# Optimization experiments

Hardware: AMD Instinct MI355X
Metric: run time of the kernel (lower is better)

The kernel has to match this reference:

```python
import jax, jax.numpy as jnp
import numpy as np

B, T, H, N = 2, 1024, 32, 64
HN = H * N              # 2048 hidden size
KVH, KVD = 8, 512       # GQA kv heads / kv width; repeat = HN // KVD = 4
LW, LA, LV, LG, LK = 64, 64, 32, 128, 32   # wavgk_split_list
EPS = 1e-6

def _rms(x, w):
    xf = x.astype(jnp.float32)
    var = jnp.mean(xf * xf, axis=-1, keepdims=True)
    return (w * (xf * jax.lax.rsqrt(var + EPS))).astype(x.dtype)

def _rot_half(x):
    x1, x2 = jnp.split(x, 2, axis=-1)
    return jnp.concatenate([-x2, x1], axis=-1)

def setup_inputs():
    key = jax.random.key(0)
    ks = iter(jax.random.split(key, 32))
    nrm = lambda s, sc=1.0: jax.random.normal(next(ks), s, jnp.float32) * sc
    d = {
        'x_in': nrm((B, T, HN)),
        'v_first': nrm((B, T, KVH, N)),
        'k_first': nrm((B, T, KVH, N)),
        'state': jnp.zeros((B, H, N, N), jnp.float32),
    }
    pos = jnp.arange(T, dtype=jnp.float32)
    inv = 1.0 / (10000.0 ** (jnp.arange(0, N, 2, dtype=jnp.float32) / N))
    ang = pos[:, None] * inv[None, :]
    ang = jnp.concatenate([ang, ang], axis=-1)   # [T, N]
    d['calc_cos'] = jnp.broadcast_to(jnp.cos(ang), (B, T, N))
    d['calc_sin'] = jnp.broadcast_to(jnp.sin(ang), (B, T, N))
    d.update(
        wavgk1=nrm((HN, LW + LA + LV + LG + LK), 0.02),
        w0=jnp.zeros((HN,), jnp.float32), w2=nrm((LW, HN), 0.02),
        a0=jnp.zeros((HN,), jnp.float32), a2=nrm((LA, HN), 0.02),
        v0=jnp.zeros((KVD,), jnp.float32), v2=nrm((LV, KVD), 0.02),
        g2=nrm((LG, HN), 0.02),
        k0=jnp.zeros((KVD,), jnp.float32), k2=nrm((LK, KVD), 0.02),
        r_k=nrm((H, N), 0.1),
        RKV_w=nrm((HN + 2 * KVD, HN), 0.02),
        O_w=nrm((HN, HN), 0.02),
        R_bias=jnp.zeros((HN,), jnp.float32),
        K_bias=jnp.zeros((KVD,), jnp.float32),
        V_bias=jnp.zeros((KVD,), jnp.float32),
        O_bias=jnp.zeros((HN,), jnp.float32),
        ln_r=jnp.ones((N,), jnp.float32),
        ln_k=jnp.ones((N,), jnp.float32),
        ln1=jnp.ones((HN,), jnp.float32),
    )
    return d

def reference(x_in, v_first, k_first, state, calc_cos, calc_sin, wavgk1, w0, w2,
              a0, a2, v0, v2, g2, k0, k2, r_k, RKV_w, O_w, R_bias, K_bias,
              V_bias, O_bias, ln_r, ln_k, ln1):
    rep = HN // KVD
    x = _rms(x_in, ln1)
    rkv = x @ RKV_w.T                                   # dense form of fpx_matmul
    r, k, v = jnp.split(rkv, [HN, HN + KVD], axis=-1)
    xw, xa, xv, xg, xk = jnp.split(x @ wavgk1, [LW, LW + LA, LW + LA + LV, LW + LA + LV + LG], axis=-1)
    r = r + R_bias; k = k + K_bias; v = v + V_bias
    r = _rms(r.reshape(B, T, H, N), ln_r)
    k = _rms(k.reshape(B, T, KVH, N), ln_k)
    cos, sin = calc_cos[:, :, None, :], calc_sin[:, :, None, :]   # unsqueeze_dim=2
    r = r * cos + _rot_half(r) * sin
    k = k * cos + _rot_half(k) * sin
    v = v.reshape(B, T, KVH, N)
    # layer_id > 0 path: gated residual toward layer-0 v/k
    gate_v = jax.nn.sigmoid(xv @ v2 + v0).reshape(B, T, KVH, N)
    v = v + (v_first - v) * gate_v
    gate_k = jax.nn.sigmoid(xk @ k2 + k0).reshape(B, T, KVH, N)
    k = k + (k_first - k) * gate_k
    w = jnp.tanh(xw) @ w2 + w0
    w = -jax.nn.softplus(-w) - 0.5
    # GQA repeat kv heads to H
    k = jnp.broadcast_to(k[:, :, :, None, :], (B, T, KVH, rep, N)).reshape(B, T, HN)
    v = jnp.broadcast_to(v[:, :, :, None, :], (B, T, KVH, rep, N)).reshape(B, T, HN)
    r = r.reshape(B, T, HN)
    a = jax.nn.sigmoid(xa @ a2 + a0)
    g = jax.nn.sigmoid(xg) @ g2
    kh = k.reshape(B, T, H, N)
    kk = (kh / jnp.maximum(jnp.linalg.norm(kh, axis=-1, keepdims=True), 1e-12)).reshape(B, T, HN)
    k = k * (1.0 - w + a)
    aa, bb = -kk, kk * a
    w = -jnp.exp(w.astype(jnp.float32))                 # log-decay (negative)
    # RWKV-7 recurrence: S <- S*diag(exp(w)) + (S a) b^T + v k^T ; o = S r
    hv = lambda t: jnp.moveaxis(t.reshape(B, T, H, N).astype(jnp.float32), 1, 0)
    def step(S, ts):
        r_t, w_t, k_t, v_t, a_t, b_t = ts               # each [B,H,N]
        sa = jnp.einsum('bhvk,bhk->bhv', S, a_t)
        S = S * jnp.exp(w_t)[:, :, None, :] + sa[..., None] * b_t[:, :, None, :] + v_t[..., None] * k_t[:, :, None, :]
        return S, jnp.einsum('bhvk,bhk->bhv', S, r_t)
    _, o = jax.lax.scan(step, state.astype(jnp.float32), (hv(r), hv(w), hv(k), hv(v), hv(aa), hv(bb)))
    xx = jnp.moveaxis(o, 0, 1).reshape(B, T, HN) * float(N) ** -0.5
    r_, k_, v_ = (t.reshape(B, T, H, N) for t in (r, k, v))
    bonus = (jnp.sum(r_ * k_ * r_k, axis=-1, keepdims=True) * v_).reshape(B, T, HN)
    xx = xx.astype(x_in.dtype) + bonus
    return x_in + (xx * g) @ O_w.T + O_bias
```

## Files before the change

### kernel.cpp

```cpp
#include <hip/hip_runtime.h>
#include <hip/hip_bf16.h>
#include <stdint.h>

#define B_ 2
#define T_ 1024
#define H_ 32
#define N_ 64
#define HN_ 2048
#define KVH_ 8
#define KVD_ 512
#define MTOK 2048
#define SMN 7168
#define KCAT 320
#define CH 64
#define NCH 16
#define NCHUNK 1024

typedef __bf16 bf16x8 __attribute__((ext_vector_type(8)));
typedef float f32x4 __attribute__((ext_vector_type(4)));

typedef __attribute__((address_space(1))) uint32_t gu32;
typedef __attribute__((address_space(3))) uint32_t lu32;
__device__ __forceinline__ void gload16(const void* g, void* l) {
    __builtin_amdgcn_global_load_lds((gu32*)g, (lu32*)l, 16, 0, 0);
}

__device__ __forceinline__ float sigmf(float x) { return 1.f / (1.f + expf(-x)); }

#define PREP_N1 (3072 * 2048)
#define PREP_N2 (2048 * 2048)
#define PREP_N3 (320 * 2048)
#define PREP_N4 (SMN * KCAT)
__global__ void prep_kernel(const float* __restrict__ RKV_w, const float* __restrict__ O_w,
                            const float* __restrict__ wavgk1,
                            const float* __restrict__ w2, const float* __restrict__ a2,
                            const float* __restrict__ v2, const float* __restrict__ g2,
                            const float* __restrict__ k2,
                            __hip_bfloat16* __restrict__ RKVb, __hip_bfloat16* __restrict__ OWb,
                            __hip_bfloat16* __restrict__ WT1b, __hip_bfloat16* __restrict__ Wcatb) {
    long i = (long)blockIdx.x * 256 + threadIdx.x;
    if (i < PREP_N1) { RKVb[i] = __float2bfloat16(RKV_w[i]); return; }
    i -= PREP_N1;
    if (i < PREP_N2) { OWb[i] = __float2bfloat16(O_w[i]); return; }
    i -= PREP_N2;
    if (i < PREP_N3) {
        int c = (int)(i / 2048), r = (int)(i % 2048);
        WT1b[i] = __float2bfloat16(wavgk1[(size_t)r * 320 + c]);
        return;
    }
    i -= PREP_N3;
    if (i >= PREP_N4) return;
    int j = (int)(i / KCAT), k = (int)(i % KCAT);
    float v = 0.f;
    if (j < 2048)      { if (k < 64)             v = w2[(size_t)k * 2048 + j]; }
    else if (j < 4096) { if (k >= 64 && k < 128)  v = a2[(size_t)(k - 64) * 2048 + (j - 2048)]; }
    else if (j < 4608) { if (k >= 128 && k < 160) v = v2[(size_t)(k - 128) * 512 + (j - 4096)]; }
    else if (j < 6656) { if (k >= 160 && k < 288) v = g2[(size_t)(k - 160) * 2048 + (j - 4608)]; }
    else               { if (k >= 288)            v = k2[(size_t)(k - 288) * 512 + (j - 6656)]; }
    Wcatb[i] = __float2bfloat16(v);
}

__global__ __launch_bounds__(256) void rmsnorm_kernel(const float* __restrict__ x,
                                                      const float* __restrict__ ln1,
                                                      __hip_bfloat16* __restrict__ out) {
    const int bt = blockIdx.x, tid = threadIdx.x;
    const float* row = x + (size_t)bt * HN_;
    float4 v0 = *(const float4*)(row + tid * 8);
    float4 v1 = *(const float4*)(row + tid * 8 + 4);
    float s = v0.x*v0.x + v0.y*v0.y + v0.z*v0.z + v0.w*v0.w
            + v1.x*v1.x + v1.y*v1.y + v1.z*v1.z + v1.w*v1.w;
    for (int m = 1; m < 64; m <<= 1) s += __shfl_xor(s, m);
    __shared__ float red[4];
    if ((tid & 63) == 0) red[tid >> 6] = s;
    __syncthreads();
    s = red[0] + red[1] + red[2] + red[3];
    float scale = rsqrtf(s * (1.f / HN_) + 1e-6f);
    float vals[8] = {v0.x, v0.y, v0.z, v0.w, v1.x, v1.y, v1.z, v1.w};
    #pragma unroll
    for (int j = 0; j < 8; ++j)
        out[(size_t)bt * HN_ + tid * 8 + j] = __float2bfloat16(vals[j] * scale * ln1[tid * 8 + j]);
}

__global__ __launch_bounds__(256) void gemm_xw_sk(const __hip_bfloat16* __restrict__ A,
                                                  const __hip_bfloat16* __restrict__ B,
                                                  float* __restrict__ Cp, int M, int N, int K) {
    __shared__ __align__(16) __hip_bfloat16 As[64][40];
    __shared__ __align__(16) __hip_bfloat16 Bs[64][40];
    const int tid = threadIdx.x;
    const int wave = tid >> 6, lane = tid & 63;
    const int wr = (wave >> 1) * 32, wc = (wave & 1) * 32;
    const int brow = blockIdx.y << 6, bcol = blockIdx.x << 6;
    const int z = blockIdx.z;
    const int kbeg = z * (K >> 2), kend = kbeg + (K >> 2);
    const int lrow = tid >> 2, lcol = (tid & 3) << 3;
    const int fr = lane & 15, ko = (lane >> 4) << 3;
    f32x4 acc[2][2] = {};
    for (int k0 = kbeg; k0 < kend; k0 += 32) {
        uint4 av = *(const uint4*)(A + (size_t)(brow + lrow) * K + k0 + lcol);
        uint4 bv = *(const uint4*)(B + (size_t)(bcol + lrow) * K + k0 + lcol);
        *(uint4*)(&As[lrow][lcol]) = av;
        *(uint4*)(&Bs[lrow][lcol]) = bv;
        __syncthreads();
        bf16x8 af0 = *(const bf16x8*)(&As[wr + fr][ko]);
        bf16x8 af1 = *(const bf16x8*)(&As[wr + 16 + fr][ko]);
        bf16x8 bf0 = *(const bf16x8*)(&Bs[wc + fr][ko]);
        bf16x8 bf1 = *(const bf16x8*)(&Bs[wc + 16 + fr][ko]);
        acc[0][0] = __builtin_amdgcn_mfma_f32_16x16x32_bf16(af0, bf0, acc[0][0], 0, 0, 0);
        acc[0][1] = __builtin_amdgcn_mfma_f32_16x16x32_bf16(af0, bf1, acc[0][1], 0, 0, 0);
        acc[1][0] = __builtin_amdgcn_mfma_f32_16x16x32_bf16(af1, bf0, acc[1][0], 0, 0, 0);
        acc[1][1] = __builtin_amdgcn_mfma_f32_16x16x32_bf16(af1, bf1, acc[1][1], 0, 0, 0);
        __syncthreads();
    }
    const int cr = (lane >> 4) << 2, cc = lane & 15;
    float* Cz = Cp + (size_t)z * M * N;
    #pragma unroll
    for (int i = 0; i < 2; ++i)
        #pragma unroll
        for (int j = 0; j < 2; ++j)
            #pragma unroll
            for (int r = 0; r < 4; ++r) {
                int row = brow + wr + i * 16 + cr + r;
                int col = bcol + wc + j * 16 + cc;
                Cz[(size_t)row * N + col] = acc[i][j][r];
            }
}

__global__ void xw_reduce(const float* __restrict__ Cp, __hip_bfloat16* __restrict__ out) {
    long i = (long)blockIdx.x * 256 + threadIdx.x;
    if (i >= (long)MTOK * KCAT) return;
    const long MN = (long)MTOK * KCAT;
    float v = Cp[i] + Cp[i + MN] + Cp[i + 2 * MN] + Cp[i + 3 * MN];
    int c = (int)(i % KCAT);
    if (c < 64) v = tanhf(v);
    else if (c >= 160 && c < 288) v = sigmf(v);
    out[i] = __float2bfloat16(v);
}

__global__ __launch_bounds__(256) void gemm_bt128(const __hip_bfloat16* __restrict__ A,
                                                  const __hip_bfloat16* __restrict__ B,
                                                  float* __restrict__ C, int M, int N, int K,
                                                  const float* __restrict__ bias,
                                                  const float* __restrict__ addend) {
    __shared__ __align__(16) __hip_bfloat16 As[128][32];
    __shared__ __align__(16) __hip_bfloat16 Bs[128][32];
    const int tid = threadIdx.x;
    const int wave = tid >> 6, lane = tid & 63;
    const int wr = (wave >> 1) * 64, wc = (wave & 1) * 64;
    const int brow = blockIdx.y << 7, bcol = blockIdx.x << 7;
    const int fr = lane & 15, ko = (lane >> 4) << 3;
    const int ar0 = wave * 32;
    const int sr = lane >> 2;
    const int sc = (lane & 3) << 3;
    f32x4 acc[4][4] = {};
    const __hip_bfloat16* gA0 = A + (size_t)(brow + ar0 + sr) * K + sc;
    const __hip_bfloat16* gA1 = A + (size_t)(brow + ar0 + 16 + sr) * K + sc;
    const __hip_bfloat16* gB0 = B + (size_t)(bcol + ar0 + sr) * K + sc;
    const __hip_bfloat16* gB1 = B + (size_t)(bcol + ar0 + 16 + sr) * K + sc;
    for (int k0 = 0; k0 < K; k0 += 32) {
        gload16(gA0 + k0, &As[ar0][0]);
        gload16(gA1 + k0, &As[ar0 + 16][0]);
        gload16(gB0 + k0, &Bs[ar0][0]);
        gload16(gB1 + k0, &Bs[ar0 + 16][0]);
        __syncthreads();
        bf16x8 af[4], bfr[4];
        #pragma unroll
        for (int i = 0; i < 4; ++i) {
            af[i]  = *(const bf16x8*)(&As[wr + i * 16 + fr][ko]);
            bfr[i] = *(const bf16x8*)(&Bs[wc + i * 16 + fr][ko]);
        }
        #pragma unroll
        for (int i = 0; i < 4; ++i)
            #pragma unroll
            for (int j = 0; j < 4; ++j)
                acc[i][j] = __builtin_amdgcn_mfma_f32_16x16x32_bf16(af[i], bfr[j], acc[i][j], 0, 0, 0);
        __syncthreads();
    }
    const int cr = (lane >> 4) << 2, cc = lane & 15;
    #pragma unroll
    for (int i = 0; i < 4; ++i)
        #pragma unroll
        for (int j = 0; j < 4; ++j) {
            const int row0 = brow + wr + i * 16 + cr;
            const int col = bcol + wc + j * 16 + cc;
            #pragma unroll
            for (int r = 0; r < 4; ++r) {
                float v = acc[i][j][r];
                if (bias) v += bias[col];
                if (addend) v += addend[(size_t)(row0 + r) * N + col];
                C[(size_t)(row0 + r) * N + col] = v;
            }
        }
}

__global__ __launch_bounds__(256) void compose_kernel(
    const float* __restrict__ RKV, const float* __restrict__ SM,
    const float* __restrict__ v_first, const float* __restrict__ k_first,
    const float* __restrict__ cosd, const float* __restrict__ sind,
    const float* __restrict__ R_bias, const float* __restrict__ K_bias,
    const float* __restrict__ V_bias, const float* __restrict__ w0,
    const float* __restrict__ a0, const float* __restrict__ v0b,
    const float* __restrict__ k0b, const float* __restrict__ ln_r,
    const float* __restrict__ ln_k, const float* __restrict__ r_k,
    char* __restrict__ SC, __hip_bfloat16* __restrict__ VB, float* __restrict__ SB,
    __hip_bfloat16* __restrict__ G) {
    __shared__ __align__(16) float rbuf[HN_];
    __shared__ __align__(16) float kbuf[KVD_];
    __shared__ __align__(16) float vbuf[KVD_];
    __shared__ float knorms[KVH_];
    __shared__ float cosb[64], sinb[64];
    const int bt = blockIdx.x;
    const int b = bt >> 10, t = bt & 1023;
    const int tid = threadIdx.x;
    const float* rkvrow = RKV + (size_t)bt * 3072;
    const float* smrow = SM + (size_t)bt * SMN;

    if (tid < 64) {
        cosb[tid] = cosd[(size_t)bt * 64 + tid];
        sinb[tid] = sind[(size_t)bt * 64 + tid];
    }

    const int h = tid >> 3;
    const int off = (tid & 7) << 3;
    const int n0 = tid << 3;
    float rraw[8];
    {
        float4 x0 = *(const float4*)(rkvrow + n0);
        float4 x1 = *(const float4*)(rkvrow + n0 + 4);
        float4 b0 = *(const float4*)(R_bias + n0);
        float4 b1 = *(const float4*)(R_bias + n0 + 4);
        rraw[0] = x0.x + b0.x; rraw[1] = x0.y + b0.y; rraw[2] = x0.z + b0.z; rraw[3] = x0.w + b0.w;
        rraw[4] = x1.x + b1.x; rraw[5] = x1.y + b1.y; rraw[6] = x1.z + b1.z; rraw[7] = x1.w + b1.w;
    }
    float rss = 0.f;
    #pragma unroll
    for (int j = 0; j < 8; ++j) { rss += rraw[j] * rraw[j]; rbuf[n0 + j] = rraw[j]; }
    rss += __shfl_xor(rss, 1); rss += __shfl_xor(rss, 2); rss += __shfl_xor(rss, 4);
    float rscale = rsqrtf(rss * (1.f / 64.f) + 1e-6f);

    const int kvh = tid >> 5;
    const int ko2 = (tid & 31) << 1;
    const int kidx = kvh * 64 + ko2;
    float kraw0 = rkvrow[2048 + kidx] + K_bias[kidx];
    float kraw1 = rkvrow[2048 + kidx + 1] + K_bias[kidx + 1];
    float kss = kraw0 * kraw0 + kraw1 * kraw1;
    kss += __shfl_xor(kss, 1); kss += __shfl_xor(kss, 2); kss += __shfl_xor(kss, 4);
    kss += __shfl_xor(kss, 8); kss += __shfl_xor(kss, 16);
    float kscale = rsqrtf(kss * (1.f / 64.f) + 1e-6f);
    kbuf[kidx] = kraw0; kbuf[kidx + 1] = kraw1;

    {
        float va = rkvrow[2560 + kidx] + V_bias[kidx];
        float vb2 = rkvrow[2560 + kidx + 1] + V_bias[kidx + 1];
        float gv0 = sigmf(smrow[4096 + kidx] + v0b[kidx]);
        float gv1 = sigmf(smrow[4096 + kidx + 1] + v0b[kidx + 1]);
        vbuf[kidx] = va + (v_first[(size_t)bt * 512 + kidx] - va) * gv0;
        vbuf[kidx + 1] = vb2 + (v_first[(size_t)bt * 512 + kidx + 1] - vb2) * gv1;
    }
    __syncthreads();

    float rf[8];
    #pragma unroll
    for (int j = 0; j < 8; ++j) {
        int nn = off + j;
        int nn2 = (nn + 32) & 63;
        float val = rbuf[h * 64 + nn] * rscale * ln_r[nn];
        float oth = rbuf[h * 64 + nn2] * rscale * ln_r[nn2];
        float rot = (nn < 32) ? -oth : oth;
        rf[j] = val * cosb[nn] + rot * sinb[nn];
    }
    float kfv[2];
    #pragma unroll
    for (int j = 0; j < 2; ++j) {
        int nn = ko2 + j;
        int nn2 = (nn + 32) & 63;
        float val = kbuf[kvh * 64 + nn] * kscale * ln_k[nn];
        float oth = kbuf[kvh * 64 + nn2] * kscale * ln_k[nn2];
        float rot = (nn < 32) ? -oth : oth;
        float kr = val * cosb[nn] + rot * sinb[nn];
        float gk = sigmf(smrow[6656 + kvh * 64 + nn] + k0b[kvh * 64 + nn]);
        kfv[j] = kr + (k_first[(size_t)bt * 512 + kvh * 64 + nn] - kr) * gk;
    }
    __syncthreads();
    kbuf[kidx] = kfv[0]; kbuf[kidx + 1] = kfv[1];
    float kn = kfv[0] * kfv[0] + kfv[1] * kfv[1];
    kn += __shfl_xor(kn, 1); kn += __shfl_xor(kn, 2); kn += __shfl_xor(kn, 4);
    kn += __shfl_xor(kn, 8); kn += __shfl_xor(kn, 16);
    if ((tid & 31) == 0) knorms[kvh] = fmaxf(sqrtf(kn), 1e-12f);
    __syncthreads();

    const float knv = knorms[h >> 2];
    char* scb = SC + ((size_t)(b * H_ + h) * T_ + t) * 896;
    __hip_bfloat16* us = (__hip_bfloat16*)scb;
    float* df = (float*)(scb + 640);
    float4 w1a = *(const float4*)(smrow + n0);
    float4 w1b = *(const float4*)(smrow + n0 + 4);
    float4 ara = *(const float4*)(smrow + 2048 + n0);
    float4 arb = *(const float4*)(smrow + 2048 + n0 + 4);
    float4 ga  = *(const float4*)(smrow + 4608 + n0);
    float4 gb  = *(const float4*)(smrow + 4608 + n0 + 4);
    float w1arr[8] = {w1a.x, w1a.y, w1a.z, w1a.w, w1b.x, w1b.y, w1b.z, w1b.w};
    float aarr[8] = {ara.x, ara.y, ara.z, ara.w, arb.x, arb.y, arb.z, arb.w};
    float garr[8] = {ga.x, ga.y, ga.z, ga.w, gb.x, gb.y, gb.z, gb.w};
    float bsum = 0.f;
    #pragma unroll
    for (int j = 0; j < 8; ++j) {
        int nn = off + j, n = n0 + j;
        float w1 = w1arr[j] + w0[n];
        float w2v = -log1pf(expf(-w1)) - 0.5f;
        float av = sigmf(aarr[j] + a0[n]);
        float dec = expf(-expf(w2v));
        float kb = kbuf[(h >> 2) * 64 + nn];
        float vbv = vbuf[(h >> 2) * 64 + nn];
        float kkv = kb / knv;
        float ksc = kb * (1.f - w2v + av);
        us[nn]       = __float2bfloat16(rf[j]);
        us[64 + nn]  = __float2bfloat16(ksc);
        us[128 + nn] = __float2bfloat16(-kkv);
        us[192 + nn] = __float2bfloat16(kkv * av);
        us[256 + nn] = __float2bfloat16(vbv);
        df[nn] = dec;
        VB[(size_t)bt * HN_ + n] = __float2bfloat16(vbv);
        G[(size_t)bt * HN_ + n] = __float2bfloat16(garr[j]);
        bsum += rf[j] * ksc * r_k[h * 64 + nn];
    }
    bsum += __shfl_xor(bsum, 1); bsum += __shfl_xor(bsum, 2); bsum += __shfl_xor(bsum, 4);
    if ((tid & 7) == 0) SB[bt * H_ + h] = bsum;
}

__global__ __launch_bounds__(256) void scan_pass1(
    const char* __restrict__ SC, float* __restrict__ Q, float* __restrict__ O,
    float* __restrict__ Pf, float* __restrict__ Sf) {
    const int chunk = blockIdx.x;
    const int bh = chunk >> 4, c = chunk & 15;
    const int b = bh >> 5, h = bh & 31;
    const int tid = threadIdx.x;
    const int wid = tid >> 6, lane = tid & 63;
    const int cq = lane >> 4;
    const int cb = cq << 4;
    const int row = (wid << 4) + (lane & 15);
    const char* base = SC + ((size_t)bh * T_ + (size_t)c * CH) * 896;
    __shared__ __align__(16) float ld[2][6][64];

    f32x4 P4[4], S4[4];
    #pragma unroll
    for (int j = 0; j < 4; ++j)
        #pragma unroll
        for (int e = 0; e < 4; ++e) {
            P4[j][e] = (cb + 4 * j + e == row) ? 1.f : 0.f;
            S4[j][e] = 0.f;
        }

    float p0 = 0.f, p1 = 0.f;
    auto LOADT = [&](int t) {
        const __hip_bfloat16* us = (const __hip_bfloat16*)(base + (size_t)t * 896);
        if (wid == 0)      { p0 = __bfloat162float(us[128 + lane]); p1 = __bfloat162float(us[lane]); }
        else if (wid == 1) { p0 = __bfloat162float(us[192 + lane]); p1 = __bfloat162float(us[256 + lane]); }
        else if (wid == 2) { p0 = *(const float*)(base + (size_t)t * 896 + 640 + 4 * lane); }
        else               { p0 = __bfloat162float(us[64 + lane]); }
    };
    LOADT(0);
    float* qrow = Q + (size_t)chunk * CH * 64 + row;
    float* orow = O + ((size_t)b * T_ + (size_t)c * CH) * HN_ + h * 64 + row;
    for (int t = 0; t < CH; ++t) {
        const int buf = t & 1;
        if (wid == 0)      { ld[buf][0][lane] = p0; ld[buf][4][lane] = p1; }
        else if (wid == 1) { ld[buf][1][lane] = p0; ld[buf][5][lane] = p1; }
        else if (wid == 2) { ld[buf][2][lane] = p0; }
        else               { ld[buf][3][lane] = p0; }
        __syncthreads();
        if (t + 1 < CH) LOADT(t + 1);
        f32x4 a4[4];
        #pragma unroll
        for (int j = 0; j < 4; ++j) a4[j] = *(const f32x4*)&ld[buf][0][cb + 4 * j];
        f32x4 dpv = {0,0,0,0}, dsv = {0,0,0,0};
        #pragma unroll
        for (int j = 0; j < 4; ++j) { dpv += P4[j] * a4[j]; dsv += S4[j] * a4[j]; }
        float dp = dpv[0] + dpv[1] + dpv[2] + dpv[3];
        float dsd = dsv[0] + dsv[1] + dsv[2] + dsv[3];
        dp += __shfl_xor(dp, 16);  dp += __shfl_xor(dp, 32);
        dsd += __shfl_xor(dsd, 16); dsd += __shfl_xor(dsd, 32);
        const float vt = ld[buf][5][row];
        const f32x4 cPv = {dp, dp, dp, dp}, sav = {dsd, dsd, dsd, dsd}, vtv = {vt, vt, vt, vt};
        f32x4 qp = {0,0,0,0}, op = {0,0,0,0};
        #pragma unroll
        for (int j = 0; j < 4; ++j) {
            f32x4 d4 = *(const f32x4*)&ld[buf][2][cb + 4 * j];
            f32x4 b4 = *(const f32x4*)&ld[buf][1][cb + 4 * j];
            f32x4 k4 = *(const f32x4*)&ld[buf][3][cb + 4 * j];
            f32x4 r4 = *(const f32x4*)&ld[buf][4][cb + 4 * j];
            f32x4 Pn = P4[j] * d4 + cPv * b4;
            f32x4 Sn = S4[j] * d4 + sav * b4 + vtv * k4;
            P4[j] = Pn; S4[j] = Sn;
            qp += Pn * r4; op += Sn * r4;
        }
        float qs = qp[0] + qp[1] + qp[2] + qp[3];
        float os = op[0] + op[1] + op[2] + op[3];
        qs += __shfl_xor(qs, 16); qs += __shfl_xor(qs, 32);
        os += __shfl_xor(os, 16); os += __shfl_xor(os, 32);
        if (cq == 0) {
            qrow[(size_t)t * 64] = qs;
            orow[(size_t)t * HN_] = os;
        }
    }
    float* pf = Pf + (size_t)chunk * 4096 + (size_t)row * 64 + cb;
    float* sf = Sf + (size_t)chunk * 4096 + (size_t)row * 64 + cb;
    #pragma unroll
    for (int j = 0; j < 4; ++j) {
        *(f32x4*)(pf + 4 * j) = P4[j];
        *(f32x4*)(sf + 4 * j) = S4[j];
    }
}

__global__ __launch_bounds__(256) void scan_pass2(
    const float* __restrict__ Pf, float* __restrict__ Sf, const float* __restrict__ state) {
    const int blk = blockIdx.x;
    const int bh = blk >> 2, rb = blk & 3;
    const int tid = threadIdx.x;
    const int lv = tid >> 4, c0 = (tid & 15) << 2;
    __shared__ __align__(16) float S[16][68];
    __shared__ __align__(16) float P[64][64];

    *(f32x4*)&S[lv][c0] = *(const f32x4*)&state[(size_t)bh * 4096 + 1024 * rb + tid * 4];
    const size_t pbase = (size_t)(bh * NCH) * 4096;
    {
        f32x4 p0[4];
        #pragma unroll
        for (int j = 0; j < 4; ++j) p0[j] = *(const f32x4*)&Pf[pbase + tid * 16 + 4 * j];
        #pragma unroll
        for (int j = 0; j < 4; ++j) *(f32x4*)(&P[0][0] + tid * 16 + 4 * j) = p0[j];
    }
    __syncthreads();

    for (int c = 0; c < NCH; ++c) {
        const size_t ck = (size_t)(bh * NCH + c) * 4096;
        f32x4 pp[4];
        if (c + 1 < NCH) {
            #pragma unroll
            for (int j = 0; j < 4; ++j) pp[j] = *(const f32x4*)&Pf[ck + 4096 + tid * 16 + 4 * j];
        }
        f32x4 acc = *(const f32x4*)&Sf[ck + 1024 * rb + tid * 4];
        f32x4 cur = *(const f32x4*)&S[lv][c0];
        #pragma unroll 4
        for (int k4 = 0; k4 < 64; k4 += 4) {
            f32x4 sk4 = *(const f32x4*)&S[lv][k4];
            #pragma unroll
            for (int kk = 0; kk < 4; ++kk) {
                f32x4 pr = *(const f32x4*)&P[k4 + kk][c0];
                f32x4 sv = {sk4[kk], sk4[kk], sk4[kk], sk4[kk]};
                acc += sv * pr;
            }
        }
        __syncthreads();
        *(f32x4*)&S[lv][c0] = acc;
        if (c + 1 < NCH) {
            #pragma unroll
            for (int j = 0; j < 4; ++j) *(f32x4*)(&P[0][0] + tid * 16 + 4 * j) = pp[j];
        }
        *(f32x4*)&Sf[ck + 1024 * rb + tid * 4] = cur;
        __syncthreads();
    }
}

__global__ __launch_bounds__(64) void pass3_post(
    const float* __restrict__ Q, const float* __restrict__ Sinit, const float* __restrict__ OL,
    const float* __restrict__ SB, const __hip_bfloat16* __restrict__ VB,
    const __hip_bfloat16* __restrict__ G, __hip_bfloat16* __restrict__ Ub) {
    const int chunk = blockIdx.x;
    const int bh = chunk >> 4, c = chunk & 15;
    const int b = bh >> 5, h = bh & 31;
    const int t = threadIdx.x;
    __shared__ __align__(16) float S[64][64];
    #pragma unroll
    for (int j = 0; j < 16; ++j)
        *(f32x4*)&S[t][4 * j] = *(const f32x4*)&Sinit[(size_t)chunk * 4096 + (size_t)t * 64 + 4 * j];
    __syncthreads();
    float q[64];
    #pragma unroll
    for (int j = 0; j < 16; ++j)
        *(f32x4*)&q[4 * j] = *(const f32x4*)&Q[((size_t)chunk * CH + t) * 64 + 4 * j];
    const size_t bt = (size_t)b * T_ + (size_t)c * CH + t;
    const float sb = SB[bt * H_ + h];
    const float* olrow = OL + bt * HN_ + h * 64;
    const __hip_bfloat16* vbrow = VB + bt * HN_ + h * 64;
    const __hip_bfloat16* grow = G + bt * HN_ + h * 64;
    __hip_bfloat16* urow = Ub + bt * HN_ + h * 64;
    #pragma unroll 4
    for (int v = 0; v < 64; ++v) {
        f32x4 a = {0, 0, 0, 0};
        #pragma unroll
        for (int j = 0; j < 16; ++j)
            a += *(const f32x4*)&S[v][4 * j] * *(const f32x4*)&q[4 * j];
        float o = (a[0] + a[1] + a[2] + a[3] + olrow[v]) * 0.125f;
        float u = (o + sb * __bfloat162float(vbrow[v])) * __bfloat162float(grow[v]);
        urow[v] = __float2bfloat16(u);
    }
}

extern "C" void kernel_launch(void* const* d_in, const int* in_sizes, int n_in,
                              void* d_out, int out_size, void* d_ws, size_t ws_size,
                              hipStream_t stream) {
    (void)in_sizes; (void)n_in; (void)out_size; (void)ws_size;
    const float* x_in    = (const float*)d_in[0];
    const float* v_first = (const float*)d_in[1];
    const float* k_first = (const float*)d_in[2];
    const float* state   = (const float*)d_in[3];
    const float* calc_cos= (const float*)d_in[4];
    const float* calc_sin= (const float*)d_in[5];
    const float* wavgk1  = (const float*)d_in[6];
    const float* w0      = (const float*)d_in[7];
    const float* w2      = (const float*)d_in[8];
    const float* a0      = (const float*)d_in[9];
    const float* a2      = (const float*)d_in[10];
    const float* v0      = (const float*)d_in[11];
    const float* v2      = (const float*)d_in[12];
    const float* g2      = (const float*)d_in[13];
    const float* k0      = (const float*)d_in[14];
    const float* k2      = (const float*)d_in[15];
    const float* r_k     = (const float*)d_in[16];
    const float* RKV_w   = (const float*)d_in[17];
    const float* O_w     = (const float*)d_in[18];
    const float* R_bias  = (const float*)d_in[19];
    const float* K_bias  = (const float*)d_in[20];
    const float* V_bias  = (const float*)d_in[21];
    const float* O_bias  = (const float*)d_in[22];
    const float* ln_r    = (const float*)d_in[23];
    const float* ln_k    = (const float*)d_in[24];
    const float* ln1     = (const float*)d_in[25];
    float* out = (float*)d_out;

    char* ws = (char*)d_ws;
    size_t off = 0;
    auto alloc = [&](size_t bytes) -> char* {
        char* p = ws + off;
        off = (off + bytes + 255) & ~(size_t)255;
        return p;
    };
    char*  SCb = alloc((size_t)64 * T_ * 896);
    __hip_bfloat16* Ub = (__hip_bfloat16*)SCb;
    __hip_bfloat16* VBb = (__hip_bfloat16*)alloc((size_t)MTOK * HN_ * 2);
    __hip_bfloat16* Gb  = (__hip_bfloat16*)alloc((size_t)MTOK * HN_ * 2);
    float* SBf = (float*)alloc((size_t)MTOK * H_ * 4);
    float* Of  = (float*)alloc((size_t)MTOK * HN_ * 4);
    __hip_bfloat16* OWb = (__hip_bfloat16*)alloc((size_t)2048 * 2048 * 2);

    size_t ovl = off;
    float* SMf = (float*)alloc((size_t)MTOK * SMN * 4);
    __hip_bfloat16* Xb     = (__hip_bfloat16*)alloc((size_t)MTOK * HN_ * 2);
    __hip_bfloat16* RKVb   = (__hip_bfloat16*)alloc((size_t)3072 * 2048 * 2);
    __hip_bfloat16* WT1b   = (__hip_bfloat16*)alloc((size_t)320 * 2048 * 2);
    __hip_bfloat16* Wcatb  = (__hip_bfloat16*)alloc((size_t)SMN * KCAT * 2);
    __hip_bfloat16* XWmodb = (__hip_bfloat16*)alloc((size_t)MTOK * KCAT * 2);
    float* RKVf  = (float*)alloc((size_t)MTOK * 3072 * 4);
    float* XWp   = (float*)alloc((size_t)4 * MTOK * KCAT * 4);
    off = ovl;
    float* Qf  = (float*)alloc((size_t)NCHUNK * CH * 64 * 4);
    float* Pff = (float*)alloc((size_t)NCHUNK * 4096 * 4);
    float* Sff = (float*)alloc((size_t)NCHUNK * 4096 * 4);

    {
        long total = (long)PREP_N1 + PREP_N2 + PREP_N3 + PREP_N4;
        prep_kernel<<<(int)((total + 255) / 256), 256, 0, stream>>>(
            RKV_w, O_w, wavgk1, w2, a2, v2, g2, k2, RKVb, OWb, WT1b, Wcatb);
    }

    rmsnorm_kernel<<<MTOK, 256, 0, stream>>>(x_in, ln1, Xb);

    gemm_bt128<<<dim3(3072 / 128, MTOK / 128), 256, 0, stream>>>(Xb, RKVb, RKVf, MTOK, 3072, 2048, nullptr, nullptr);
    gemm_xw_sk<<<dim3(KCAT / 64, MTOK / 64, 4), 256, 0, stream>>>(Xb, WT1b, XWp, MTOK, KCAT, 2048);
    xw_reduce<<<(MTOK * KCAT + 255) / 256, 256, 0, stream>>>(XWp, XWmodb);
    gemm_bt128<<<dim3(SMN / 128, MTOK / 128), 256, 0, stream>>>(XWmodb, Wcatb, SMf, MTOK, SMN, KCAT, nullptr, nullptr);

    compose_kernel<<<MTOK, 256, 0, stream>>>(RKVf, SMf, v_first, k_first, calc_cos, calc_sin,
                                             R_bias, K_bias, V_bias, w0, a0, v0, k0,
                                             ln_r, ln_k, r_k, SCb, VBb, SBf, Gb);

    scan_pass1<<<NCHUNK, 256, 0, stream>>>(SCb, Qf, Of, Pff, Sff);
    scan_pass2<<<B_ * H_ * 4, 256, 0, stream>>>(Pff, Sff, state);
    pass3_post<<<NCHUNK, 64, 0, stream>>>(Qf, Sff, Of, SBf, VBb, Gb, Ub);

    gemm_bt128<<<dim3(HN_ / 128, MTOK / 128), 256, 0, stream>>>(Ub, OWb, out, MTOK, HN_, 2048, O_bias, x_in);
}
```

Before: 420.7 us.

## Shrink scan pass1 to one wave per chunk with four state rows per lane

```diff
diff --git a/kernel.cpp b/kernel.cpp
--- a/kernel.cpp
+++ b/kernel.cpp
@@ -327,88 +327,118 @@
     if ((tid & 7) == 0) SB[bt * H_ + h] = bsum;
 }
 
-__global__ __launch_bounds__(256) void scan_pass1(
+__global__ __launch_bounds__(64, 1) void scan_pass1(
     const char* __restrict__ SC, float* __restrict__ Q, float* __restrict__ O,
     float* __restrict__ Pf, float* __restrict__ Sf) {
     const int chunk = blockIdx.x;
     const int bh = chunk >> 4, c = chunk & 15;
     const int b = bh >> 5, h = bh & 31;
-    const int tid = threadIdx.x;
-    const int wid = tid >> 6, lane = tid & 63;
+    const int lane = threadIdx.x;
+    const int g = lane & 15;
     const int cq = lane >> 4;
     const int cb = cq << 4;
-    const int row = (wid << 4) + (lane & 15);
+    const int r0 = g << 2;
     const char* base = SC + ((size_t)bh * T_ + (size_t)c * CH) * 896;
-    __shared__ __align__(16) float ld[2][6][64];
-
-    f32x4 P4[4], S4[4];
-    #pragma unroll
-    for (int j = 0; j < 4; ++j)
-        #pragma unroll
-        for (int e = 0; e < 4; ++e) {
-            P4[j][e] = (cb + 4 * j + e == row) ? 1.f : 0.f;
-            S4[j][e] = 0.f;
-        }
-
-    float p0 = 0.f, p1 = 0.f;
+    __shared__ __align__(16) float ld[6][64];
+
+    f32x4 P4[4][4], S4[4][4];
+    #pragma unroll
+    for (int i = 0; i < 4; ++i)
+        #pragma unroll
+        for (int j = 0; j < 4; ++j)
+            #pragma unroll
+            for (int e = 0; e < 4; ++e) {
+                P4[i][j][e] = (cb + 4 * j + e == r0 + i) ? 1.f : 0.f;
+                S4[i][j][e] = 0.f;
+            }
+
+    float pa, pb, pd, pk, pr, pv;
     auto LOADT = [&](int t) {
         const __hip_bfloat16* us = (const __hip_bfloat16*)(base + (size_t)t * 896);
-        if (wid == 0)      { p0 = __bfloat162float(us[128 + lane]); p1 = __bfloat162float(us[lane]); }
-        else if (wid == 1) { p0 = __bfloat162float(us[192 + lane]); p1 = __bfloat162float(us[256 + lane]); }
-        else if (wid == 2) { p0 = *(const float*)(base + (size_t)t * 896 + 640 + 4 * lane); }
-        else               { p0 = __bfloat162float(us[64 + lane]); }
+        pr = __bfloat162float(us[lane]);
+        pk = __bfloat162float(us[64 + lane]);
+        pa = __bfloat162float(us[128 + lane]);
+        pb = __bfloat162float(us[192 + lane]);
+        pv = __bfloat162float(us[256 + lane]);
+        pd = *(const float*)(base + (size_t)t * 896 + 640 + 4 * lane);
     };
     LOADT(0);
-    float* qrow = Q + (size_t)chunk * CH * 64 + row;
-    float* orow = O + ((size_t)b * T_ + (size_t)c * CH) * HN_ + h * 64 + row;
+    float* qbase = Q + (size_t)chunk * CH * 64 + r0;
+    float* obase = O + ((size_t)b * T_ + (size_t)c * CH) * HN_ + h * 64 + r0;
     for (int t = 0; t < CH; ++t) {
-        const int buf = t & 1;
-        if (wid == 0)      { ld[buf][0][lane] = p0; ld[buf][4][lane] = p1; }
-        else if (wid == 1) { ld[buf][1][lane] = p0; ld[buf][5][lane] = p1; }
-        else if (wid == 2) { ld[buf][2][lane] = p0; }
-        else               { ld[buf][3][lane] = p0; }
+        ld[0][lane] = pa; ld[1][lane] = pb; ld[2][lane] = pd;
+        ld[3][lane] = pk; ld[4][lane] = pr; ld[5][lane] = pv;
         __syncthreads();
         if (t + 1 < CH) LOADT(t + 1);
-        f32x4 a4[4];
-        #pragma unroll
-        for (int j = 0; j < 4; ++j) a4[j] = *(const f32x4*)&ld[buf][0][cb + 4 * j];
-        f32x4 dpv = {0,0,0,0}, dsv = {0,0,0,0};
-        #pragma unroll
-        for (int j = 0; j < 4; ++j) { dpv += P4[j] * a4[j]; dsv += S4[j] * a4[j]; }
-        float dp = dpv[0] + dpv[1] + dpv[2] + dpv[3];
-        float dsd = dsv[0] + dsv[1] + dsv[2] + dsv[3];
-        dp += __shfl_xor(dp, 16);  dp += __shfl_xor(dp, 32);
-        dsd += __shfl_xor(dsd, 16); dsd += __shfl_xor(dsd, 32);
-        const float vt = ld[buf][5][row];
-        const f32x4 cPv = {dp, dp, dp, dp}, sav = {dsd, dsd, dsd, dsd}, vtv = {vt, vt, vt, vt};
-        f32x4 qp = {0,0,0,0}, op = {0,0,0,0};
+        f32x4 dpv[4] = {{0,0,0,0},{0,0,0,0},{0,0,0,0},{0,0,0,0}};
+        f32x4 dsv[4] = {{0,0,0,0},{0,0,0,0},{0,0,0,0},{0,0,0,0}};
         #pragma unroll
         for (int j = 0; j < 4; ++j) {
-            f32x4 d4 = *(const f32x4*)&ld[buf][2][cb + 4 * j];
-            f32x4 b4 = *(const f32x4*)&ld[buf][1][cb + 4 * j];
-            f32x4 k4 = *(const f32x4*)&ld[buf][3][cb + 4 * j];
-            f32x4 r4 = *(const f32x4*)&ld[buf][4][cb + 4 * j];
-            f32x4 Pn = P4[j] * d4 + cPv * b4;
-            f32x4 Sn = S4[j] * d4 + sav * b4 + vtv * k4;
-            P4[j] = Pn; S4[j] = Sn;
-            qp += Pn * r4; op += Sn * r4;
-        }
-        float qs = qp[0] + qp[1] + qp[2] + qp[3];
-        float os = op[0] + op[1] + op[2] + op[3];
-        qs += __shfl_xor(qs, 16); qs += __shfl_xor(qs, 32);
-        os += __shfl_xor(os, 16); os += __shfl_xor(os, 32);
+            f32x4 a4 = *(const f32x4*)&ld[0][cb + 4 * j];
+            #pragma unroll
+            for (int i = 0; i < 4; ++i) {
+                dpv[i] += P4[i][j] * a4;
+                dsv[i] += S4[i][j] * a4;
+            }
+        }
+        f32x4 dp, dsd;
+        #pragma unroll
+        for (int i = 0; i < 4; ++i) {
+            dp[i]  = dpv[i][0] + dpv[i][1] + dpv[i][2] + dpv[i][3];
+            dsd[i] = dsv[i][0] + dsv[i][1] + dsv[i][2] + dsv[i][3];
+        }
+        #pragma unroll
+        for (int e = 0; e < 4; ++e) {
+            dp[e]  += __shfl_xor(dp[e], 16);  dp[e]  += __shfl_xor(dp[e], 32);
+            dsd[e] += __shfl_xor(dsd[e], 16); dsd[e] += __shfl_xor(dsd[e], 32);
+        }
+        const f32x4 vt4 = *(const f32x4*)&ld[5][r0];
+        f32x4 qacc[4] = {{0,0,0,0},{0,0,0,0},{0,0,0,0},{0,0,0,0}};
+        f32x4 oacc[4] = {{0,0,0,0},{0,0,0,0},{0,0,0,0},{0,0,0,0}};
+        #pragma unroll
+        for (int j = 0; j < 4; ++j) {
+            f32x4 d4 = *(const f32x4*)&ld[2][cb + 4 * j];
+            f32x4 b4 = *(const f32x4*)&ld[1][cb + 4 * j];
+            f32x4 k4 = *(const f32x4*)&ld[3][cb + 4 * j];
+            f32x4 r4 = *(const f32x4*)&ld[4][cb + 4 * j];
+            #pragma unroll
+            for (int i = 0; i < 4; ++i) {
+                f32x4 dpb = {dp[i], dp[i], dp[i], dp[i]};
+                f32x4 dsb = {dsd[i], dsd[i], dsd[i], dsd[i]};
+                f32x4 vtb = {vt4[i], vt4[i], vt4[i], vt4[i]};
+                f32x4 Pn = P4[i][j] * d4 + dpb * b4;
+                f32x4 Sn = S4[i][j] * d4 + dsb * b4 + vtb * k4;
+                P4[i][j] = Pn; S4[i][j] = Sn;
+                qacc[i] += Pn * r4;
+                oacc[i] += Sn * r4;
+            }
+        }
+        f32x4 qv, ov;
+        #pragma unroll
+        for (int i = 0; i < 4; ++i) {
+            qv[i] = qacc[i][0] + qacc[i][1] + qacc[i][2] + qacc[i][3];
+            ov[i] = oacc[i][0] + oacc[i][1] + oacc[i][2] + oacc[i][3];
+        }
+        #pragma unroll
+        for (int e = 0; e < 4; ++e) {
+            qv[e] += __shfl_xor(qv[e], 16); qv[e] += __shfl_xor(qv[e], 32);
+            ov[e] += __shfl_xor(ov[e], 16); ov[e] += __shfl_xor(ov[e], 32);
+        }
         if (cq == 0) {
-            qrow[(size_t)t * 64] = qs;
-            orow[(size_t)t * HN_] = os;
-        }
-    }
-    float* pf = Pf + (size_t)chunk * 4096 + (size_t)row * 64 + cb;
-    float* sf = Sf + (size_t)chunk * 4096 + (size_t)row * 64 + cb;
-    #pragma unroll
-    for (int j = 0; j < 4; ++j) {
-        *(f32x4*)(pf + 4 * j) = P4[j];
-        *(f32x4*)(sf + 4 * j) = S4[j];
-    }
+            *(f32x4*)(qbase + (size_t)t * 64) = qv;
+            *(f32x4*)(obase + (size_t)t * HN_) = ov;
+        }
+        __syncthreads();
+    }
+    float* pf = Pf + (size_t)chunk * 4096 + (size_t)r0 * 64 + cb;
+    float* sf = Sf + (size_t)chunk * 4096 + (size_t)r0 * 64 + cb;
+    #pragma unroll
+    for (int i = 0; i < 4; ++i)
+        #pragma unroll
+        for (int j = 0; j < 4; ++j) {
+            *(f32x4*)(pf + (size_t)i * 64 + 4 * j) = P4[i][j];
+            *(f32x4*)(sf + (size_t)i * 64 + 4 * j) = S4[i][j];
+        }
 }
 
 __global__ __launch_bounds__(256) void scan_pass2(
@@ -574,7 +604,7 @@
                                              R_bias, K_bias, V_bias, w0, a0, v0, k0,
                                              ln_r, ln_k, r_k, SCb, VBb, SBf, Gb);
 
-    scan_pass1<<<NCHUNK, 256, 0, stream>>>(SCb, Qf, Of, Pff, Sff);
+    scan_pass1<<<NCHUNK, 64, 0, stream>>>(SCb, Qf, Of, Pff, Sff);
     scan_pass2<<<B_ * H_ * 4, 256, 0, stream>>>(Pff, Sff, state);
     pass3_post<<<NCHUNK, 64, 0, stream>>>(Qf, Sff, Of, SBf, VBb, Gb, Ub);
 
```

New measurement: 452.4 us. 7.5% more time.

## Vectorize bf16 stores and remap GEMM workgroups across XCDs

Applied to the files above, without the earlier changes.

```diff
diff --git a/kernel.cpp b/kernel.cpp
--- a/kernel.cpp
+++ b/kernel.cpp
@@ -76,9 +76,11 @@
     s = red[0] + red[1] + red[2] + red[3];
     float scale = rsqrtf(s * (1.f / HN_) + 1e-6f);
     float vals[8] = {v0.x, v0.y, v0.z, v0.w, v1.x, v1.y, v1.z, v1.w};
+    __align__(16) __hip_bfloat16 tmp[8];
     #pragma unroll
     for (int j = 0; j < 8; ++j)
-        out[(size_t)bt * HN_ + tid * 8 + j] = __float2bfloat16(vals[j] * scale * ln1[tid * 8 + j]);
+        tmp[j] = __float2bfloat16(vals[j] * scale * ln1[tid * 8 + j]);
+    *(uint4*)&out[(size_t)bt * HN_ + tid * 8] = *(const uint4*)tmp;
 }
 
 __global__ __launch_bounds__(256) void gemm_xw_sk(const __hip_bfloat16* __restrict__ A,
@@ -143,10 +145,15 @@
                                                   const float* __restrict__ addend) {
     __shared__ __align__(16) __hip_bfloat16 As[128][32];
     __shared__ __align__(16) __hip_bfloat16 Bs[128][32];
+    const int nwg = gridDim.x;
+    int wg = blockIdx.x;
+    wg = (wg & 7) * (nwg >> 3) + (wg >> 3);
+    const int nx = N >> 7;
+    const int bx = wg % nx, by = wg / nx;
+    const int brow = by << 7, bcol = bx << 7;
     const int tid = threadIdx.x;
     const int wave = tid >> 6, lane = tid & 63;
     const int wr = (wave >> 1) * 64, wc = (wave & 1) * 64;
-    const int brow = blockIdx.y << 7, bcol = blockIdx.x << 7;
     const int fr = lane & 15, ko = (lane >> 4) << 3;
     const int ar0 = wave * 32;
     const int sr = lane >> 2;
@@ -301,6 +308,8 @@
     float w1arr[8] = {w1a.x, w1a.y, w1a.z, w1a.w, w1b.x, w1b.y, w1b.z, w1b.w};
     float aarr[8] = {ara.x, ara.y, ara.z, ara.w, arb.x, arb.y, arb.z, arb.w};
     float garr[8] = {ga.x, ga.y, ga.z, ga.w, gb.x, gb.y, gb.z, gb.w};
+    __align__(16) __hip_bfloat16 t_r[8], t_k[8], t_a[8], t_b[8], t_v[8], t_vb[8], t_g[8];
+    __align__(16) float t_d[8];
     float bsum = 0.f;
     #pragma unroll
     for (int j = 0; j < 8; ++j) {
@@ -313,16 +322,25 @@
         float vbv = vbuf[(h >> 2) * 64 + nn];
         float kkv = kb / knv;
         float ksc = kb * (1.f - w2v + av);
-        us[nn]       = __float2bfloat16(rf[j]);
-        us[64 + nn]  = __float2bfloat16(ksc);
-        us[128 + nn] = __float2bfloat16(-kkv);
-        us[192 + nn] = __float2bfloat16(kkv * av);
-        us[256 + nn] = __float2bfloat16(vbv);
-        df[nn] = dec;
-        VB[(size_t)bt * HN_ + n] = __float2bfloat16(vbv);
-        G[(size_t)bt * HN_ + n] = __float2bfloat16(garr[j]);
+        t_r[j] = __float2bfloat16(rf[j]);
+        t_k[j] = __float2bfloat16(ksc);
+        t_a[j] = __float2bfloat16(-kkv);
+        t_b[j] = __float2bfloat16(kkv * av);
+        t_v[j] = __float2bfloat16(vbv);
+        t_d[j] = dec;
+        t_vb[j] = __float2bfloat16(vbv);
+        t_g[j] = __float2bfloat16(garr[j]);
         bsum += rf[j] * ksc * r_k[h * 64 + nn];
     }
+    *(uint4*)&us[off]        = *(const uint4*)t_r;
+    *(uint4*)&us[64 + off]   = *(const uint4*)t_k;
+    *(uint4*)&us[128 + off]  = *(const uint4*)t_a;
+    *(uint4*)&us[192 + off]  = *(const uint4*)t_b;
+    *(uint4*)&us[256 + off]  = *(const uint4*)t_v;
+    *(float4*)&df[off]       = *(const float4*)&t_d[0];
+    *(float4*)&df[off + 4]   = *(const float4*)&t_d[4];
+    *(uint4*)&VB[(size_t)bt * HN_ + n0] = *(const uint4*)t_vb;
+    *(uint4*)&G[(size_t)bt * HN_ + n0]  = *(const uint4*)t_g;
     bsum += __shfl_xor(bsum, 1); bsum += __shfl_xor(bsum, 2); bsum += __shfl_xor(bsum, 4);
     if ((tid & 7) == 0) SB[bt * H_ + h] = bsum;
 }
@@ -565,10 +583,10 @@
 
     rmsnorm_kernel<<<MTOK, 256, 0, stream>>>(x_in, ln1, Xb);
 
-    gemm_bt128<<<dim3(3072 / 128, MTOK / 128), 256, 0, stream>>>(Xb, RKVb, RKVf, MTOK, 3072, 2048, nullptr, nullptr);
+    gemm_bt128<<<(3072 / 128) * (MTOK / 128), 256, 0, stream>>>(Xb, RKVb, RKVf, MTOK, 3072, 2048, nullptr, nullptr);
     gemm_xw_sk<<<dim3(KCAT / 64, MTOK / 64, 4), 256, 0, stream>>>(Xb, WT1b, XWp, MTOK, KCAT, 2048);
     xw_reduce<<<(MTOK * KCAT + 255) / 256, 256, 0, stream>>>(XWp, XWmodb);
-    gemm_bt128<<<dim3(SMN / 128, MTOK / 128), 256, 0, stream>>>(XWmodb, Wcatb, SMf, MTOK, SMN, KCAT, nullptr, nullptr);
+    gemm_bt128<<<(SMN / 128) * (MTOK / 128), 256, 0, stream>>>(XWmodb, Wcatb, SMf, MTOK, SMN, KCAT, nullptr, nullptr);
 
     compose_kernel<<<MTOK, 256, 0, stream>>>(RKVf, SMf, v_first, k_first, calc_cos, calc_sin,
                                              R_bias, K_bias, V_bias, w0, a0, v0, k0,
@@ -578,5 +596,5 @@
     scan_pass2<<<B_ * H_ * 4, 256, 0, stream>>>(Pff, Sff, state);
     pass3_post<<<NCHUNK, 64, 0, stream>>>(Qf, Sff, Of, SBf, VBb, Gb, Ub);
 
-    gemm_bt128<<<dim3(HN_ / 128, MTOK / 128), 256, 0, stream>>>(Ub, OWb, out, MTOK, HN_, 2048, O_bias, x_in);
-}
+    gemm_bt128<<<(HN_ / 128) * (MTOK / 128), 256, 0, stream>>>(Ub, OWb, out, MTOK, HN_, 2048, O_bias, x_in);
+}
```

Result: no change. 412.8 us (-1.9%).
